# Kernel optimization log

Measured on AMD Instinct MI355X. Metric: run time of the kernel, lower is better.

The kernel has to match this reference:

```python
import jax, jax.numpy as jnp
import numpy as np

N_NODES = 50000
N_EDGES = 200000
C_IN = 128
C_MID = 128
NNZ = 2 * N_EDGES  # each 1-simplex (edge) touches exactly 2 nodes


def setup_inputs() -> dict:
    key = jax.random.key(0)
    k1, k2, k3, k4 = jax.random.split(key, 4)
    x = jax.random.normal(k1, (N_EDGES, C_IN), dtype=jnp.float32)
    # xavier-style scale for weights
    w1 = jax.random.normal(k2, (C_IN, C_MID), dtype=jnp.float32) * (1.0 / np.sqrt(C_IN))
    w2 = jax.random.normal(k3, (C_MID, C_MID), dtype=jnp.float32) * (1.0 / np.sqrt(C_MID))
    # COO incidence B_1 [n_nodes, n_edges]: edge j is incident to 2 random nodes
    inc_rows = jax.random.randint(k4, (NNZ,), 0, N_NODES, dtype=jnp.int32)
    inc_cols = (jnp.arange(NNZ, dtype=jnp.int32) // 2).astype(jnp.int32)
    return {
        "x": x,
        "w1": w1,
        "w2": w2,
        "inc_rows": inc_rows,
        "inc_cols": inc_cols,
        "n_nodes": N_NODES,
        "n_edges": N_EDGES,
    }


def reference(x, w1, w2, inc_rows, inc_cols, n_nodes, n_edges):
    # Layer 1 (edges -> nodes): h = relu(B_1 @ (x @ W1)), no aggregation norm
    xw = x @ w1                                    # [n_edges, c_mid]
    msg = xw[inc_cols]                             # gather per nonzero [nnz, c_mid]
    h = jax.ops.segment_sum(msg, inc_rows, num_segments=n_nodes)  # [n_nodes, c_mid]
    h = jax.nn.relu(h)
    # Layer 2 (nodes -> edges): y = sigmoid(norm(B_1^T @ (h @ W2)))
    hw = h @ w2                                    # [n_nodes, c_mid]
    msg2 = hw[inc_rows]                            # [nnz, c_mid]
    y = jax.ops.segment_sum(msg2, inc_cols, num_segments=n_edges)  # [n_edges, c_mid]
    deg = jax.ops.segment_sum(jnp.ones((inc_cols.shape[0],), dtype=y.dtype),
                              inc_cols, num_segments=n_edges)      # row sums of B_1^T
    y = y / deg[:, None]
    y = jax.nn.sigmoid(y)
    # torch.mean(y, dim=0)[0] -> scalar (first channel of the per-channel mean)
    return jnp.mean(y, axis=0)[0]
```

## Files before the change

### kernel.cpp

```cpp
#include <hip/hip_runtime.h>
#include <hip/hip_bf16.h>

#define N_NODES 50000
#define N_EDGES 200000
#define CCH 128
#define SLOT_CAP 32
#define N_PAD 50048

typedef __attribute__((ext_vector_type(8))) short short8;
typedef __attribute__((ext_vector_type(4))) float f32x4;

__device__ inline ushort f2bf(float f) {
    union { __hip_bfloat16 h; ushort u; } cv;
    cv.h = __float2bfloat16(f);
    return cv.u;
}

__global__ void prep_fill_kernel(const float* __restrict__ w1, const float* __restrict__ w2,
                                 const int* __restrict__ inc_rows,
                                 ushort* __restrict__ w1t, float* __restrict__ w2c0,
                                 int* __restrict__ cnt, int* __restrict__ slots) {
    int idx = blockIdx.x * 256 + threadIdx.x;
    if (idx < CCH * CCH) {
        int n = idx >> 7, k = idx & 127;
        w1t[idx] = f2bf(w1[k * CCH + n]);
    }
    if (idx < CCH) w2c0[idx] = w2[idx * CCH];
    if (idx < 2 * N_EDGES) {
        int n = inc_rows[idx];
        int slot = atomicAdd(&cnt[n], 1);
        if (slot < SLOT_CAP) slots[n * SLOT_CAP + slot] = idx >> 1;
    }
}

__launch_bounds__(256)
__global__ void agg_kernel(const float* __restrict__ x,
                           const int* __restrict__ cnt,
                           const int* __restrict__ slots,
                           ushort* __restrict__ xs) {
    int gw = (blockIdx.x * 256 + threadIdx.x) >> 6;
    int l = threadIdx.x & 63;
    int wid  = gw >> 1;
    int half = gw & 1;
    int ch   = half * 64 + l;
    if (wid >= N_NODES) {
        xs[(size_t)wid * CCH + ch] = 0;
        return;
    }
    int ev  = slots[(size_t)wid * SLOT_CAP + (l & (SLOT_CAP - 1))];
    int deg = min(cnt[wid], SLOT_CAP);

    const float* xc = x + ch;
    float a0 = 0.f, a1 = 0.f, a2 = 0.f, a3 = 0.f;
    float a4 = 0.f, a5 = 0.f, a6 = 0.f, a7 = 0.f;
    int i = 0;
    for (; i + 7 < deg; i += 8) {
        int e0 = __shfl(ev, i),     e1 = __shfl(ev, i + 1);
        int e2 = __shfl(ev, i + 2), e3 = __shfl(ev, i + 3);
        int e4 = __shfl(ev, i + 4), e5 = __shfl(ev, i + 5);
        int e6 = __shfl(ev, i + 6), e7 = __shfl(ev, i + 7);
        a0 += xc[(size_t)e0 * CCH];
        a1 += xc[(size_t)e1 * CCH];
        a2 += xc[(size_t)e2 * CCH];
        a3 += xc[(size_t)e3 * CCH];
        a4 += xc[(size_t)e4 * CCH];
        a5 += xc[(size_t)e5 * CCH];
        a6 += xc[(size_t)e6 * CCH];
        a7 += xc[(size_t)e7 * CCH];
    }
    for (; i + 1 < deg; i += 2) {
        int e0 = __shfl(ev, i), e1 = __shfl(ev, i + 1);
        a0 += xc[(size_t)e0 * CCH];
        a1 += xc[(size_t)e1 * CCH];
    }
    if (i < deg) {
        int e0 = __shfl(ev, i);
        a0 += xc[(size_t)e0 * CCH];
    }
    a0 += a1; a2 += a3; a4 += a5; a6 += a7;
    a0 += a2; a4 += a6;
    a0 += a4;
    xs[(size_t)wid * CCH + ch] = f2bf(a0);
}

__launch_bounds__(256)
__global__ void gemm2_kernel(const ushort* __restrict__ xs,
                             const ushort* __restrict__ w1t,
                             const float* __restrict__ w2c0,
                             float* __restrict__ hw0) {
    __shared__ ushort lds_x[64 * CCH];
    __shared__ ushort lds_w[CCH * CCH];
    __shared__ float  lds_w2[CCH];
    const int tid = threadIdx.x;
    const int base = blockIdx.x * 64;

    char* ldsw_c = reinterpret_cast<char*>(lds_w);
    for (int c = tid; c < 2048; c += 256) {
        int n = c >> 4, kc = c & 15;
        int4 v = *reinterpret_cast<const int4*>(w1t + c * 8);
        int byte_in = (kc * 16) ^ ((n & 7) << 4);
        *reinterpret_cast<int4*>(ldsw_c + n * 256 + byte_in) = v;
    }
    char* ldsx_c = reinterpret_cast<char*>(lds_x);
    for (int c = tid; c < 1024; c += 256) {
        int r = c >> 4, kc = c & 15;
        int4 v = *reinterpret_cast<const int4*>(xs + (size_t)(base + r) * CCH + kc * 8);
        int byte_in = (kc * 16) ^ ((r & 7) << 4);
        *reinterpret_cast<int4*>(ldsx_c + r * 256 + byte_in) = v;
    }
    if (tid < CCH) lds_w2[tid] = w2c0[tid];
    __syncthreads();

    const int w  = tid >> 6;
    const int l  = tid & 63;
    const int lr = l & 15;
    const int lq = l >> 4;

    short8 af[4];
    {
        int row = w * 16 + lr;
#pragma unroll
        for (int ks = 0; ks < 4; ks++) {
            int byte_in = (ks * 64 + lq * 16) ^ ((row & 7) << 4);
            af[ks] = *reinterpret_cast<short8*>(ldsx_c + row * 256 + byte_in);
        }
    }

    f32x4 acc[8];
#pragma unroll
    for (int cf = 0; cf < 8; cf++) acc[cf] = (f32x4){0.f, 0.f, 0.f, 0.f};

#pragma unroll
    for (int cf = 0; cf < 8; cf++) {
        int row = cf * 16 + lr;
#pragma unroll
        for (int ks = 0; ks < 4; ks++) {
            int byte_in = (ks * 64 + lq * 16) ^ ((row & 7) << 4);
            short8 b = *reinterpret_cast<short8*>(ldsw_c + row * 256 + byte_in);
            acc[cf] = __builtin_amdgcn_mfma_f32_16x16x32_bf16(af[ks], b, acc[cf], 0, 0, 0);
        }
    }

    float part[4] = {0.f, 0.f, 0.f, 0.f};
#pragma unroll
    for (int cf = 0; cf < 8; cf++) {
        float wv = lds_w2[cf * 16 + lr];
#pragma unroll
        for (int r = 0; r < 4; r++) part[r] += fmaxf(acc[cf][r], 0.f) * wv;
    }
#pragma unroll
    for (int mask = 1; mask < 16; mask <<= 1)
#pragma unroll
        for (int r = 0; r < 4; r++) part[r] += __shfl_xor(part[r], mask);
    if (lr == 0) {
#pragma unroll
        for (int r = 0; r < 4; r++) hw0[base + w * 16 + lq * 4 + r] = part[r];
    }
}

__global__ void final_kernel(const int2* __restrict__ incp, const float* __restrict__ hw0,
                             float* __restrict__ out) {
    __shared__ float red[4];
    float s = 0.f;
    for (int e = blockIdx.x * 256 + threadIdx.x; e < N_EDGES; e += gridDim.x * 256) {
        int2 nd = incp[e];
        float z = 0.5f * (hw0[nd.x] + hw0[nd.y]);
        s += 1.f / (1.f + __expf(-z));
    }
#pragma unroll
    for (int off = 32; off; off >>= 1) s += __shfl_down(s, off);
    int l = threadIdx.x & 63, w = threadIdx.x >> 6;
    if (l == 0) red[w] = s;
    __syncthreads();
    if (threadIdx.x == 0) {
        float t = red[0] + red[1] + red[2] + red[3];
        atomicAdd(out, t * (1.0f / N_EDGES));
    }
}

extern "C" void kernel_launch(void* const* d_in, const int* in_sizes, int n_in,
                              void* d_out, int out_size, void* d_ws, size_t ws_size,
                              hipStream_t stream) {
    const float* x    = (const float*)d_in[0];
    const float* w1   = (const float*)d_in[1];
    const float* w2   = (const float*)d_in[2];
    const int*   rows = (const int*)d_in[3];
    const int2*  incp = (const int2*)d_in[3];

    char* ws = (char*)d_ws;
    int*    slots = (int*)ws;
    ushort* xs    = (ushort*)(ws + 6400000);
    int*    cnt   = (int*)(ws + 19212288);
    ushort* w1t   = (ushort*)(ws + 19412288);
    float*  w2c0  = (float*)(ws + 19445056);
    float*  hw0   = (float*)(ws + 19445568);

    hipMemsetAsync(cnt, 0, (size_t)N_NODES * sizeof(int), stream);
    hipMemsetAsync(d_out, 0, sizeof(float), stream);

    prep_fill_kernel<<<(2 * N_EDGES + 255) / 256, 256, 0, stream>>>(w1, w2, rows, w1t, w2c0, cnt, slots);
    agg_kernel<<<2 * N_PAD / 4, 256, 0, stream>>>(x, cnt, slots, xs);
    gemm2_kernel<<<N_PAD / 64, 256, 0, stream>>>(xs, w1t, w2c0, hw0);
    final_kernel<<<512, 256, 0, stream>>>(incp, hw0, (float*)d_out);
}
```

Measured before the change: 225.9 us.

## Reorder to GEMM-first over edges, then gather bf16 projected rows per node

Computes x@W1 for all edges first in an MFMA kernel that converts x to bf16 and writes a bf16 projected matrix. Then one wavefront per node gathers its incident projected rows (two channels per lane), applies relu, and dots with the first column of W2. This replaces the fp32 gather followed by a small GEMM. It halves the bytes per gathered row and makes the large x read sequential, at the cost of four times more GEMM work and an extra intermediate buffer write.

```diff
diff --git a/kernel.cpp b/kernel.cpp
--- a/kernel.cpp
+++ b/kernel.cpp
@@ -5,7 +5,6 @@
 #define N_EDGES 200000
 #define CCH 128
 #define SLOT_CAP 32
-#define N_PAD 50048
 
 typedef __attribute__((ext_vector_type(8))) short short8;
 typedef __attribute__((ext_vector_type(4))) float f32x4;
@@ -15,6 +14,8 @@
     cv.h = __float2bfloat16(f);
     return cv.u;
 }
+__device__ inline float bflo(uint u) { union { uint i; float f; } c; c.i = u << 16;        return c.f; }
+__device__ inline float bfhi(uint u) { union { uint i; float f; } c; c.i = u & 0xffff0000u; return c.f; }
 
 __global__ void prep_fill_kernel(const float* __restrict__ w1, const float* __restrict__ w2,
                                  const int* __restrict__ inc_rows,
@@ -34,128 +35,128 @@
 }
 
 __launch_bounds__(256)
-__global__ void agg_kernel(const float* __restrict__ x,
-                           const int* __restrict__ cnt,
-                           const int* __restrict__ slots,
-                           ushort* __restrict__ xs) {
-    int gw = (blockIdx.x * 256 + threadIdx.x) >> 6;
+__global__ void gemm1_kernel(const float* __restrict__ x,
+                             const ushort* __restrict__ w1t,
+                             ushort* __restrict__ xw) {
+    __shared__ ushort lds_x[64 * CCH];
+    __shared__ ushort lds_w[CCH * CCH];
+    const int tid = threadIdx.x;
+    const int base = blockIdx.x * 64;
+
+    char* ldsw_c = reinterpret_cast<char*>(lds_w);
+    for (int c = tid; c < 2048; c += 256) {
+        int n = c >> 4, kc = c & 15;
+        int4 v = *reinterpret_cast<const int4*>(w1t + c * 8);
+        int byte_in = (kc * 16) ^ ((n & 7) << 4);
+        *reinterpret_cast<int4*>(ldsw_c + n * 256 + byte_in) = v;
+    }
+    char* ldsx_c = reinterpret_cast<char*>(lds_x);
+    for (int c = tid; c < 1024; c += 256) {
+        int r = c >> 4, kc = c & 15;
+        const float* src = x + (size_t)(base + r) * CCH + kc * 8;
+        float4 f0 = *reinterpret_cast<const float4*>(src);
+        float4 f1 = *reinterpret_cast<const float4*>(src + 4);
+        int4 p;
+        p.x = (int)f2bf(f0.x) | ((int)f2bf(f0.y) << 16);
+        p.y = (int)f2bf(f0.z) | ((int)f2bf(f0.w) << 16);
+        p.z = (int)f2bf(f1.x) | ((int)f2bf(f1.y) << 16);
+        p.w = (int)f2bf(f1.z) | ((int)f2bf(f1.w) << 16);
+        int byte_in = (kc * 16) ^ ((r & 7) << 4);
+        *reinterpret_cast<int4*>(ldsx_c + r * 256 + byte_in) = p;
+    }
+    __syncthreads();
+
+    const int w  = tid >> 6;
+    const int l  = tid & 63;
+    const int lr = l & 15;
+    const int lq = l >> 4;
+
+    short8 af[4];
+    {
+        int row = w * 16 + lr;
+#pragma unroll
+        for (int ks = 0; ks < 4; ks++) {
+            int byte_in = (ks * 64 + lq * 16) ^ ((row & 7) << 4);
+            af[ks] = *reinterpret_cast<short8*>(ldsx_c + row * 256 + byte_in);
+        }
+    }
+
+    f32x4 acc[8];
+#pragma unroll
+    for (int cf = 0; cf < 8; cf++) acc[cf] = (f32x4){0.f, 0.f, 0.f, 0.f};
+
+#pragma unroll
+    for (int cf = 0; cf < 8; cf++) {
+        int row = cf * 16 + lr;
+#pragma unroll
+        for (int ks = 0; ks < 4; ks++) {
+            int byte_in = (ks * 64 + lq * 16) ^ ((row & 7) << 4);
+            short8 b = *reinterpret_cast<short8*>(ldsw_c + row * 256 + byte_in);
+            acc[cf] = __builtin_amdgcn_mfma_f32_16x16x32_bf16(af[ks], b, acc[cf], 0, 0, 0);
+        }
+    }
+
+    __syncthreads();
+#pragma unroll
+    for (int cf = 0; cf < 8; cf++) {
+#pragma unroll
+        for (int r = 0; r < 4; r++) {
+            lds_x[(w * 16 + lq * 4 + r) * CCH + cf * 16 + lr] = f2bf(acc[cf][r]);
+        }
+    }
+    __syncthreads();
+    const int4* ls = reinterpret_cast<const int4*>(lds_x);
+    int4* gd = reinterpret_cast<int4*>(xw + (size_t)base * CCH);
+#pragma unroll
+    for (int k = 0; k < 4; k++) gd[k * 256 + tid] = ls[k * 256 + tid];
+}
+
+__launch_bounds__(256)
+__global__ void gather_finish(const ushort* __restrict__ xw,
+                              const int* __restrict__ cnt,
+                              const int* __restrict__ slots,
+                              const float* __restrict__ w2c0,
+                              float* __restrict__ hw0) {
+    int wid = (blockIdx.x * 256 + threadIdx.x) >> 6;
     int l = threadIdx.x & 63;
-    int wid  = gw >> 1;
-    int half = gw & 1;
-    int ch   = half * 64 + l;
-    if (wid >= N_NODES) {
-        xs[(size_t)wid * CCH + ch] = 0;
-        return;
-    }
     int ev  = slots[(size_t)wid * SLOT_CAP + (l & (SLOT_CAP - 1))];
     int deg = min(cnt[wid], SLOT_CAP);
 
-    const float* xc = x + ch;
-    float a0 = 0.f, a1 = 0.f, a2 = 0.f, a3 = 0.f;
-    float a4 = 0.f, a5 = 0.f, a6 = 0.f, a7 = 0.f;
+    const uint* xwu = reinterpret_cast<const uint*>(xw) + l;
+    float a0 = 0.f, a1 = 0.f, b0 = 0.f, b1 = 0.f;
+    float c0 = 0.f, c1 = 0.f, d0 = 0.f, d1 = 0.f;
     int i = 0;
     for (; i + 7 < deg; i += 8) {
         int e0 = __shfl(ev, i),     e1 = __shfl(ev, i + 1);
         int e2 = __shfl(ev, i + 2), e3 = __shfl(ev, i + 3);
         int e4 = __shfl(ev, i + 4), e5 = __shfl(ev, i + 5);
         int e6 = __shfl(ev, i + 6), e7 = __shfl(ev, i + 7);
-        a0 += xc[(size_t)e0 * CCH];
-        a1 += xc[(size_t)e1 * CCH];
-        a2 += xc[(size_t)e2 * CCH];
-        a3 += xc[(size_t)e3 * CCH];
-        a4 += xc[(size_t)e4 * CCH];
-        a5 += xc[(size_t)e5 * CCH];
-        a6 += xc[(size_t)e6 * CCH];
-        a7 += xc[(size_t)e7 * CCH];
+        uint u0 = xwu[(size_t)e0 * 64], u1 = xwu[(size_t)e1 * 64];
+        uint u2 = xwu[(size_t)e2 * 64], u3 = xwu[(size_t)e3 * 64];
+        uint u4 = xwu[(size_t)e4 * 64], u5 = xwu[(size_t)e5 * 64];
+        uint u6 = xwu[(size_t)e6 * 64], u7 = xwu[(size_t)e7 * 64];
+        a0 += bflo(u0); a1 += bfhi(u0); b0 += bflo(u1); b1 += bfhi(u1);
+        c0 += bflo(u2); c1 += bfhi(u2); d0 += bflo(u3); d1 += bfhi(u3);
+        a0 += bflo(u4); a1 += bfhi(u4); b0 += bflo(u5); b1 += bfhi(u5);
+        c0 += bflo(u6); c1 += bfhi(u6); d0 += bflo(u7); d1 += bfhi(u7);
     }
     for (; i + 1 < deg; i += 2) {
         int e0 = __shfl(ev, i), e1 = __shfl(ev, i + 1);
-        a0 += xc[(size_t)e0 * CCH];
-        a1 += xc[(size_t)e1 * CCH];
+        uint u0 = xwu[(size_t)e0 * 64], u1 = xwu[(size_t)e1 * 64];
+        a0 += bflo(u0); a1 += bfhi(u0); b0 += bflo(u1); b1 += bfhi(u1);
     }
     if (i < deg) {
         int e0 = __shfl(ev, i);
-        a0 += xc[(size_t)e0 * CCH];
-    }
-    a0 += a1; a2 += a3; a4 += a5; a6 += a7;
-    a0 += a2; a4 += a6;
-    a0 += a4;
-    xs[(size_t)wid * CCH + ch] = f2bf(a0);
-}
-
-__launch_bounds__(256)
-__global__ void gemm2_kernel(const ushort* __restrict__ xs,
-                             const ushort* __restrict__ w1t,
-                             const float* __restrict__ w2c0,
-                             float* __restrict__ hw0) {
-    __shared__ ushort lds_x[64 * CCH];
-    __shared__ ushort lds_w[CCH * CCH];
-    __shared__ float  lds_w2[CCH];
-    const int tid = threadIdx.x;
-    const int base = blockIdx.x * 64;
-
-    char* ldsw_c = reinterpret_cast<char*>(lds_w);
-    for (int c = tid; c < 2048; c += 256) {
-        int n = c >> 4, kc = c & 15;
-        int4 v = *reinterpret_cast<const int4*>(w1t + c * 8);
-        int byte_in = (kc * 16) ^ ((n & 7) << 4);
-        *reinterpret_cast<int4*>(ldsw_c + n * 256 + byte_in) = v;
-    }
-    char* ldsx_c = reinterpret_cast<char*>(lds_x);
-    for (int c = tid; c < 1024; c += 256) {
-        int r = c >> 4, kc = c & 15;
-        int4 v = *reinterpret_cast<const int4*>(xs + (size_t)(base + r) * CCH + kc * 8);
-        int byte_in = (kc * 16) ^ ((r & 7) << 4);
-        *reinterpret_cast<int4*>(ldsx_c + r * 256 + byte_in) = v;
-    }
-    if (tid < CCH) lds_w2[tid] = w2c0[tid];
-    __syncthreads();
-
-    const int w  = tid >> 6;
-    const int l  = tid & 63;
-    const int lr = l & 15;
-    const int lq = l >> 4;
-
-    short8 af[4];
-    {
-        int row = w * 16 + lr;
-#pragma unroll
-        for (int ks = 0; ks < 4; ks++) {
-            int byte_in = (ks * 64 + lq * 16) ^ ((row & 7) << 4);
-            af[ks] = *reinterpret_cast<short8*>(ldsx_c + row * 256 + byte_in);
-        }
-    }
-
-    f32x4 acc[8];
-#pragma unroll
-    for (int cf = 0; cf < 8; cf++) acc[cf] = (f32x4){0.f, 0.f, 0.f, 0.f};
-
-#pragma unroll
-    for (int cf = 0; cf < 8; cf++) {
-        int row = cf * 16 + lr;
-#pragma unroll
-        for (int ks = 0; ks < 4; ks++) {
-            int byte_in = (ks * 64 + lq * 16) ^ ((row & 7) << 4);
-            short8 b = *reinterpret_cast<short8*>(ldsw_c + row * 256 + byte_in);
-            acc[cf] = __builtin_amdgcn_mfma_f32_16x16x32_bf16(af[ks], b, acc[cf], 0, 0, 0);
-        }
-    }
-
-    float part[4] = {0.f, 0.f, 0.f, 0.f};
-#pragma unroll
-    for (int cf = 0; cf < 8; cf++) {
-        float wv = lds_w2[cf * 16 + lr];
-#pragma unroll
-        for (int r = 0; r < 4; r++) part[r] += fmaxf(acc[cf][r], 0.f) * wv;
-    }
-#pragma unroll
-    for (int mask = 1; mask < 16; mask <<= 1)
-#pragma unroll
-        for (int r = 0; r < 4; r++) part[r] += __shfl_xor(part[r], mask);
-    if (lr == 0) {
-#pragma unroll
-        for (int r = 0; r < 4; r++) hw0[base + w * 16 + lq * 4 + r] = part[r];
-    }
+        uint u0 = xwu[(size_t)e0 * 64];
+        a0 += bflo(u0); a1 += bfhi(u0);
+    }
+    float h0 = fmaxf((a0 + b0) + (c0 + d0), 0.f);
+    float h1 = fmaxf((a1 + b1) + (c1 + d1), 0.f);
+    float2 wv = reinterpret_cast<const float2*>(w2c0)[l];
+    float part = h0 * wv.x + h1 * wv.y;
+#pragma unroll
+    for (int off = 32; off; off >>= 1) part += __shfl_xor(part, off);
+    if (l == 0) hw0[wid] = part;
 }
 
 __global__ void final_kernel(const int2* __restrict__ incp, const float* __restrict__ hw0,
@@ -189,17 +190,17 @@
 
     char* ws = (char*)d_ws;
     int*    slots = (int*)ws;
-    ushort* xs    = (ushort*)(ws + 6400000);
-    int*    cnt   = (int*)(ws + 19212288);
-    ushort* w1t   = (ushort*)(ws + 19412288);
-    float*  w2c0  = (float*)(ws + 19445056);
-    float*  hw0   = (float*)(ws + 19445568);
+    ushort* xw    = (ushort*)(ws + 6400000);
+    int*    cnt   = (int*)(ws + 57600000);
+    ushort* w1t   = (ushort*)(ws + 57800000);
+    float*  w2c0  = (float*)(ws + 57832768);
+    float*  hw0   = (float*)(ws + 57833280);
 
     hipMemsetAsync(cnt, 0, (size_t)N_NODES * sizeof(int), stream);
     hipMemsetAsync(d_out, 0, sizeof(float), stream);
 
     prep_fill_kernel<<<(2 * N_EDGES + 255) / 256, 256, 0, stream>>>(w1, w2, rows, w1t, w2c0, cnt, slots);
-    agg_kernel<<<2 * N_PAD / 4, 256, 0, stream>>>(x, cnt, slots, xs);
-    gemm2_kernel<<<N_PAD / 64, 256, 0, stream>>>(xs, w1t, w2c0, hw0);
+    gemm1_kernel<<<N_EDGES / 64, 256, 0, stream>>>(x, w1t, xw);
+    gather_finish<<<N_NODES / 4, 256, 0, stream>>>(xw, cnt, slots, w2c0, hw0);
     final_kernel<<<512, 256, 0, stream>>>(incp, hw0, (float*)d_out);
 }
```

Result: slower. 230.7 us (+2.1%).
